# Kernel tuning notes

Hardware: AMD Instinct MI355X
Metric: run time of the kernel (lower is better)

Reference implementation:

```python
import jax, jax.numpy as jnp
import numpy as np

B = 65536
IN_F = 1024
OUT_F = 1024


def setup_inputs() -> dict:
    key = jax.random.key(0)
    k1, k2 = jax.random.split(key)
    x = jax.random.normal(k1, (B, IN_F), dtype=jnp.float32)
    # init matches torch: normal(0, sqrt(2/(in+out)))
    std = np.sqrt(2.0 / (IN_F + OUT_F)).astype(np.float32)
    weight = jax.random.normal(k2, (OUT_F, IN_F), dtype=jnp.float32) * std
    bias = jnp.zeros((OUT_F,), dtype=jnp.float32)
    return {"x": x, "weight": weight, "bias": bias}


def reference(x, weight, bias):
    # Deterministic binarization: sign(w) in {-1, 0, +1} (sign(0)=0, same as torch)
    w_bin = jnp.sign(weight)
    # [B, in] @ [in, out] + [out]
    return jnp.matmul(x, w_bin.T) + bias[None, :]
```

## Files before the change

kernel.cpp:

```cpp
#include <hip/hip_runtime.h>


typedef __bf16 bf16x8 __attribute__((ext_vector_type(8)));
typedef float  f32x4  __attribute__((ext_vector_type(4)));

constexpr int Mdim = 65536, Ndim = 1024, Kdim = 1024;
constexpr int BM = 128, BN = 256, BK = 32;
constexpr int NKT = Kdim / BK;
constexpr int NWG = (Mdim / BM) * (Ndim / BN);
constexpr int AROWB = 80;

typedef const __attribute__((address_space(1))) char ga_char;
typedef __attribute__((address_space(3))) char lds_char;
__device__ __forceinline__ void gload16(const void* g, void* l) {
    __builtin_amdgcn_global_load_lds((ga_char*)g, (lds_char*)l, 16, 0, 0);
}
__device__ __forceinline__ f32x4 mfma16(bf16x8 a, bf16x8 b, f32x4 c) {
    return __builtin_amdgcn_mfma_f32_16x16x32_bf16(a, b, c, 0, 0, 0);
}

__global__ __launch_bounds__(256)
void wprep_kernel(const float* __restrict__ W, __bf16* __restrict__ WS) {
    const int id   = blockIdx.x * 256 + threadIdx.x;
    const int colb = id >> 15;
    const int kt   = (id >> 10) & 31;
    const int g    = id & 1023;
    const int nb   = g >> 6;
    const int lane = g & 63;
    const int row  = colb * 256 + nb * 16 + (lane & 15);
    const int col  = kt * 32 + (lane >> 4) * 8;
    const float* src = W + (size_t)row * Kdim + col;
    f32x4 a = *(const f32x4*)src;
    f32x4 b = *(const f32x4*)(src + 4);
    bf16x8 o;
#pragma unroll
    for (int e = 0; e < 4; ++e) {
        o[e]     = (__bf16)(float)((a[e] > 0.f) - (a[e] < 0.f));
        o[e + 4] = (__bf16)(float)((b[e] > 0.f) - (b[e] < 0.f));
    }
    *(bf16x8*)(WS + (size_t)id * 8) = o;
}

__global__ __launch_bounds__(512, 4)
void binlin128x256(const float* __restrict__ X, const __bf16* __restrict__ WS,
                   const float* __restrict__ bias, float* __restrict__ out)
{
    __shared__ __align__(16) char Al[2][BM * AROWB];
    __shared__ __align__(16) __bf16 Bl[2][BN * BK];

    const int swz  = (blockIdx.x & 7) * (NWG / 8) + (blockIdx.x >> 3);
    const int colb = swz & 3;
    const int rowb = swz >> 2;
    const int row0 = rowb * BM;

    const int tid  = threadIdx.x;
    const int lane = tid & 63;
    const int wid  = tid >> 6;
    const int wr   = wid >> 2;
    const int wcn  = wid & 3;
    const int fr   = lane & 15;
    const int hq   = lane >> 4;

    const int a_r = tid >> 2;
    const int a_c = (tid & 3) * 8;
    const float* Xb = X + (size_t)(row0 + a_r) * Kdim + a_c;

    const __bf16* WSb = WS + (size_t)colb * (Ndim / BN == 4 ? 262144 : 262144);

    f32x4 ra[2];
    auto GLA = [&](int kt) {
        const float* p = Xb + kt * BK;
        ra[0] = *(const f32x4*)p;
        ra[1] = *(const f32x4*)(p + 4);
    };
    auto DSWA = [&](int buf) {
        bf16x8 v;
#pragma unroll
        for (int e = 0; e < 4; ++e) {
            v[e]     = (__bf16)ra[0][e];
            v[e + 4] = (__bf16)ra[1][e];
        }
        *(bf16x8*)(&Al[buf][a_r * AROWB + a_c * 2]) = v;
    };
    auto GLB = [&](int buf, int kt) {
        const __bf16* s = WSb + (size_t)kt * 8192 + wid * 1024 + lane * 8;
        gload16(s,       &Bl[buf][wid * 1024]);
        gload16(s + 512, &Bl[buf][wid * 1024 + 512]);
    };

    auto lda = [&](int buf, int i) -> bf16x8 {
        const int row = wr * 64 + i * 16 + fr;
        return *(const bf16x8*)(&Al[buf][row * AROWB + hq * 16]);
    };
    auto ldb = [&](int buf, int j) -> bf16x8 {
        const int nb = wcn * 4 + j;
        return *(const bf16x8*)(&Bl[buf][nb * 512 + lane * 8]);
    };

    f32x4 acc[4][4] = {};

    GLA(0); GLB(0, 0); DSWA(0);
    __syncthreads();

    int cur = 0;
    for (int t = 0; t < NKT; ++t) {
        const int nxt = cur ^ 1;
        const bool pre = (t + 1 < NKT);
        if (pre) { GLA(t + 1); GLB(nxt, t + 1); }

        bf16x8 af[4];
#pragma unroll
        for (int i = 0; i < 4; ++i) af[i] = lda(cur, i);
        __builtin_amdgcn_s_setprio(1);
#pragma unroll
        for (int j = 0; j < 4; ++j) {
            bf16x8 bf = ldb(cur, j);
#pragma unroll
            for (int i = 0; i < 4; ++i)
                acc[i][j] = mfma16(af[i], bf, acc[i][j]);
        }
        __builtin_amdgcn_s_setprio(0);

        if (pre) {
            DSWA(nxt);
            __syncthreads();
        }
        cur = nxt;
    }

    const int orow = row0 + wr * 64 + hq * 4;
    const int ocol = colb * BN + wcn * 64 + fr;
#pragma unroll
    for (int j = 0; j < 4; ++j) {
        const float bv = bias[ocol + j * 16];
#pragma unroll
        for (int i = 0; i < 4; ++i)
#pragma unroll
            for (int r = 0; r < 4; ++r)
                out[(size_t)(orow + i * 16 + r) * Ndim + (ocol + j * 16)] =
                    acc[i][j][r] + bv;
    }
}

__global__ __launch_bounds__(256)
void binlin_fallback(const float* __restrict__ X, const float* __restrict__ Wf,
                     const float* __restrict__ bias, float* __restrict__ out)
{
    __shared__ __align__(16) __bf16 Al[2][128][32];
    __shared__ __align__(16) __bf16 Bl[2][128][32];
    constexpr int NT = Kdim / 32;
    const int swz  = (blockIdx.x & 7) * (4096 / 8) + (blockIdx.x >> 3);
    const int colb = swz & 7, rowb = swz >> 3;
    const int row0 = rowb * 128, col0 = colb * 128;
    const int tid = threadIdx.x, lane = tid & 63, wid = tid >> 6;
    const int wr = wid >> 1, wc = wid & 1;
    const int sr = tid >> 2, sc = (tid & 3) * 8;
    const float* Xb = X + (size_t)row0 * Kdim;
    const float* Wb = Wf + (size_t)col0 * Kdim;
    f32x4 ra[2][2], rb[2][2];
    auto GL = [&](int k0) {
#pragma unroll
        for (int p = 0; p < 2; ++p) {
            const float* sa = Xb + (size_t)(p * 64 + sr) * Kdim + k0 + sc;
            ra[p][0] = *(const f32x4*)sa; ra[p][1] = *(const f32x4*)(sa + 4);
            const float* sb = Wb + (size_t)(p * 64 + sr) * Kdim + k0 + sc;
            rb[p][0] = *(const f32x4*)sb; rb[p][1] = *(const f32x4*)(sb + 4);
        }
    };
    auto DSW = [&](int buf) {
#pragma unroll
        for (int p = 0; p < 2; ++p) {
            bf16x8 va, vb;
#pragma unroll
            for (int e = 0; e < 4; ++e) {
                va[e] = (__bf16)ra[p][0][e]; va[e + 4] = (__bf16)ra[p][1][e];
                float a = rb[p][0][e], b = rb[p][1][e];
                vb[e] = (__bf16)(float)((a > 0.f) - (a < 0.f));
                vb[e + 4] = (__bf16)(float)((b > 0.f) - (b < 0.f));
            }
            *(bf16x8*)&Al[buf][p * 64 + sr][sc] = va;
            *(bf16x8*)&Bl[buf][p * 64 + sr][sc] = vb;
        }
    };
    f32x4 acc[4][4] = {};
    const int fr = lane & 15, ks = (lane >> 4) * 8;
    auto COMP = [&](int buf) {
        bf16x8 af[4], bf[4];
#pragma unroll
        for (int i = 0; i < 4; ++i) af[i] = *(const bf16x8*)&Al[buf][wr * 64 + fr + i * 16][ks];
#pragma unroll
        for (int j = 0; j < 4; ++j) bf[j] = *(const bf16x8*)&Bl[buf][wc * 64 + fr + j * 16][ks];
#pragma unroll
        for (int i = 0; i < 4; ++i)
#pragma unroll
            for (int j = 0; j < 4; ++j)
                acc[i][j] = mfma16(af[i], bf[j], acc[i][j]);
    };
    GL(0); DSW(0); __syncthreads();
    int cur = 0;
    for (int t = 0; t < NT; ++t) {
        if (t + 1 < NT) GL((t + 1) * 32);
        COMP(cur);
        if (t + 1 < NT) { DSW(cur ^ 1); __syncthreads(); cur ^= 1; }
    }
    const int orow = row0 + wr * 64 + (lane >> 4) * 4;
    const int ocol = col0 + wc * 64 + fr;
#pragma unroll
    for (int j = 0; j < 4; ++j) {
        const float bv = bias[ocol + j * 16];
#pragma unroll
        for (int i = 0; i < 4; ++i)
#pragma unroll
            for (int r = 0; r < 4; ++r)
                out[(size_t)(orow + i * 16 + r) * Ndim + (ocol + j * 16)] = acc[i][j][r] + bv;
    }
}

extern "C" void kernel_launch(void* const* d_in, const int* in_sizes, int n_in,
                              void* d_out, int out_size, void* d_ws, size_t ws_size,
                              hipStream_t stream) {
    const float* x  = (const float*)d_in[0];
    const float* w  = (const float*)d_in[1];
    const float* b  = (const float*)d_in[2];
    float* out      = (float*)d_out;

    constexpr size_t WS_BYTES = (size_t)Ndim * Kdim * sizeof(__bf16);

    if (ws_size >= WS_BYTES) {
        __bf16* ws = (__bf16*)d_ws;
        wprep_kernel<<<dim3(512), dim3(256), 0, stream>>>(w, ws);
        binlin128x256<<<dim3(NWG), dim3(512), 0, stream>>>(x, ws, b, out);
    } else {
        binlin_fallback<<<dim3(4096), dim3(256), 0, stream>>>(x, w, b, out);
    }
}
```

Before: 233.5 us.

## Prefetch X two tiles ahead and store A in MFMA fragment order

The A operand (X rows) is now loaded from global memory two k-tiles ahead into a double register stage, while B is still fetched one tile ahead through direct-to-LDS loads. The end-of-iteration __syncthreads is replaced by explicit waitcnt on LDS and on vector memory (leaving two loads outstanding), plus a raw s_barrier, so the X prefetch can stay in flight across the barrier. The A tile in LDS moves from a padded row layout to MFMA fragment order, so each lane reads one contiguous 16-byte chunk. The extra register stage raises register pressure, and the hand-written vmcnt value depends on the compiler's load ordering, which makes correctness fragile.

```diff
diff --git a/kernel.cpp b/kernel.cpp
--- a/kernel.cpp
+++ b/kernel.cpp
@@ -8,7 +8,6 @@
 constexpr int BM = 128, BN = 256, BK = 32;
 constexpr int NKT = Kdim / BK;
 constexpr int NWG = (Mdim / BM) * (Ndim / BN);
-constexpr int AROWB = 80;
 
 typedef const __attribute__((address_space(1))) char ga_char;
 typedef __attribute__((address_space(3))) char lds_char;
@@ -18,6 +17,9 @@
 __device__ __forceinline__ f32x4 mfma16(bf16x8 a, bf16x8 b, f32x4 c) {
     return __builtin_amdgcn_mfma_f32_16x16x32_bf16(a, b, c, 0, 0, 0);
 }
+#define SBARRIER()   asm volatile("s_barrier" ::: "memory")
+#define WAIT_LGKM0() asm volatile("s_waitcnt lgkmcnt(0)" ::: "memory")
+#define WAIT_VM2()   asm volatile("s_waitcnt vmcnt(2)" ::: "memory")
 
 __global__ __launch_bounds__(256)
 void wprep_kernel(const float* __restrict__ W, __bf16* __restrict__ WS) {
@@ -42,10 +44,10 @@
 }
 
 __global__ __launch_bounds__(512, 4)
-void binlin128x256(const float* __restrict__ X, const __bf16* __restrict__ WS,
-                   const float* __restrict__ bias, float* __restrict__ out)
+void binlin_d2(const float* __restrict__ X, const __bf16* __restrict__ WS,
+               const float* __restrict__ bias, float* __restrict__ out)
 {
-    __shared__ __align__(16) char Al[2][BM * AROWB];
+    __shared__ __align__(16) __bf16 Al[2][BM * BK];
     __shared__ __align__(16) __bf16 Bl[2][BN * BK];
 
     const int swz  = (blockIdx.x & 7) * (NWG / 8) + (blockIdx.x >> 3);
@@ -61,26 +63,25 @@
     const int fr   = lane & 15;
     const int hq   = lane >> 4;
 
-    const int a_r = tid >> 2;
-    const int a_c = (tid & 3) * 8;
-    const float* Xb = X + (size_t)(row0 + a_r) * Kdim + a_c;
-
-    const __bf16* WSb = WS + (size_t)colb * (Ndim / BN == 4 ? 262144 : 262144);
-
-    f32x4 ra[2];
-    auto GLA = [&](int kt) {
-        const float* p = Xb + kt * BK;
-        ra[0] = *(const f32x4*)p;
-        ra[1] = *(const f32x4*)(p + 4);
-    };
-    auto DSWA = [&](int buf) {
+    const float* Xs = X + (size_t)(row0 + wid * 16 + fr) * Kdim + hq * 8;
+    const int a_dst = (wid * 64 + lane) * 8;
+
+    const __bf16* WSb = WS + (size_t)colb * 262144;
+
+    f32x4 rA[2][2];
+    auto GLA = [&](int kt, int s) {
+        const float* p = Xs + kt * BK;
+        rA[s][0] = *(const f32x4*)p;
+        rA[s][1] = *(const f32x4*)(p + 4);
+    };
+    auto DSWA = [&](int buf, int s) {
         bf16x8 v;
 #pragma unroll
         for (int e = 0; e < 4; ++e) {
-            v[e]     = (__bf16)ra[0][e];
-            v[e + 4] = (__bf16)ra[1][e];
-        }
-        *(bf16x8*)(&Al[buf][a_r * AROWB + a_c * 2]) = v;
+            v[e]     = (__bf16)rA[s][0][e];
+            v[e + 4] = (__bf16)rA[s][1][e];
+        }
+        *(bf16x8*)(&Al[buf][a_dst]) = v;
     };
     auto GLB = [&](int buf, int kt) {
         const __bf16* s = WSb + (size_t)kt * 8192 + wid * 1024 + lane * 8;
@@ -89,24 +90,28 @@
     };
 
     auto lda = [&](int buf, int i) -> bf16x8 {
-        const int row = wr * 64 + i * 16 + fr;
-        return *(const bf16x8*)(&Al[buf][row * AROWB + hq * 16]);
+        return *(const bf16x8*)(&Al[buf][((wr * 4 + i) * 64 + lane) * 8]);
     };
     auto ldb = [&](int buf, int j) -> bf16x8 {
-        const int nb = wcn * 4 + j;
-        return *(const bf16x8*)(&Bl[buf][nb * 512 + lane * 8]);
+        return *(const bf16x8*)(&Bl[buf][((wcn * 4 + j) * 64 + lane) * 8]);
     };
 
     f32x4 acc[4][4] = {};
 
-    GLA(0); GLB(0, 0); DSWA(0);
+    GLB(0, 0);
+    GLA(0, 0);
+    GLA(1, 1);
+    DSWA(0, 0);
     __syncthreads();
 
-    int cur = 0;
     for (int t = 0; t < NKT; ++t) {
+        const int cur = t & 1;
         const int nxt = cur ^ 1;
-        const bool pre = (t + 1 < NKT);
-        if (pre) { GLA(t + 1); GLB(nxt, t + 1); }
+        const int tB  = (t + 1 < NKT) ? t + 1 : NKT - 1;
+        const int tA  = (t + 2 < NKT) ? t + 2 : NKT - 1;
+
+        GLB(nxt, tB);
+        GLA(tA, cur);
 
         bf16x8 af[4];
 #pragma unroll
@@ -121,11 +126,11 @@
         }
         __builtin_amdgcn_s_setprio(0);
 
-        if (pre) {
-            DSWA(nxt);
-            __syncthreads();
-        }
-        cur = nxt;
+        DSWA(nxt, nxt);
+        WAIT_LGKM0();
+        WAIT_VM2();
+        __builtin_amdgcn_sched_barrier(0);
+        SBARRIER();
     }
 
     const int orow = row0 + wr * 64 + hq * 4;
@@ -229,7 +234,7 @@
     if (ws_size >= WS_BYTES) {
         __bf16* ws = (__bf16*)d_ws;
         wprep_kernel<<<dim3(512), dim3(256), 0, stream>>>(w, ws);
-        binlin128x256<<<dim3(NWG), dim3(512), 0, stream>>>(x, ws, b, out);
+        binlin_d2<<<dim3(NWG), dim3(512), 0, stream>>>(x, ws, b, out);
     } else {
         binlin_fallback<<<dim3(4096), dim3(256), 0, stream>>>(x, w, b, out);
     }
```

Result: slower. 246.6 us (+5.6%).

## Pre-convert X to bf16 MFMA layout and use 256x256 four-stage ring GEMM

Applied to the files above, without the earlier changes.

Adds an xprep kernel that converts X to bf16 in a fragment-ordered layout, so the main GEMM can stream both operands with global_load_lds straight into LDS. The new main kernel uses 256x256 tiles, a 4-slot LDS ring with prefetch depth 3, and split-phase barriers. This removes the in-loop fp32 register loads and conversion of X and raises arithmetic intensity per tile. In exchange it adds a full extra pass that reads the fp32 X and writes a bf16 copy (128 MB workspace), and it lowers occupancy to 2 workgroups per CU.

```diff
diff --git a/kernel.cpp b/kernel.cpp
--- a/kernel.cpp
+++ b/kernel.cpp
@@ -5,10 +5,9 @@
 typedef float  f32x4  __attribute__((ext_vector_type(4)));
 
 constexpr int Mdim = 65536, Ndim = 1024, Kdim = 1024;
-constexpr int BM = 128, BN = 256, BK = 32;
+constexpr int BM = 256, BN = 256, BK = 32;
 constexpr int NKT = Kdim / BK;
 constexpr int NWG = (Mdim / BM) * (Ndim / BN);
-constexpr int AROWB = 80;
 
 typedef const __attribute__((address_space(1))) char ga_char;
 typedef __attribute__((address_space(3))) char lds_char;
@@ -20,38 +19,55 @@
 }
 
 __global__ __launch_bounds__(256)
-void wprep_kernel(const float* __restrict__ W, __bf16* __restrict__ WS) {
+void xprep_kernel(const float* __restrict__ X, __bf16* __restrict__ XB) {
     const int id   = blockIdx.x * 256 + threadIdx.x;
-    const int colb = id >> 15;
+    const int l    = id & 63;
+    const int mb   = (id >> 6) & 15;
     const int kt   = (id >> 10) & 31;
-    const int g    = id & 1023;
-    const int nb   = g >> 6;
-    const int lane = g & 63;
-    const int row  = colb * 256 + nb * 16 + (lane & 15);
-    const int col  = kt * 32 + (lane >> 4) * 8;
-    const float* src = W + (size_t)row * Kdim + col;
+    const int rowb = id >> 15;
+    const float* src = X + (size_t)(rowb * 256 + mb * 16 + (l & 15)) * Kdim
+                         + kt * 32 + (l >> 4) * 8;
     f32x4 a = *(const f32x4*)src;
     f32x4 b = *(const f32x4*)(src + 4);
     bf16x8 o;
 #pragma unroll
     for (int e = 0; e < 4; ++e) {
+        o[e]     = (__bf16)a[e];
+        o[e + 4] = (__bf16)b[e];
+    }
+    *(bf16x8*)(XB + (size_t)id * 8) = o;
+}
+
+__global__ __launch_bounds__(256)
+void wprep_kernel(const float* __restrict__ W, __bf16* __restrict__ WB) {
+    const int id   = blockIdx.x * 256 + threadIdx.x;
+    const int l    = id & 63;
+    const int nb   = (id >> 6) & 15;
+    const int kt   = (id >> 10) & 31;
+    const int colb = id >> 15;
+    const float* src = W + (size_t)(colb * 256 + nb * 16 + (l & 15)) * Kdim
+                         + kt * 32 + (l >> 4) * 8;
+    f32x4 a = *(const f32x4*)src;
+    f32x4 b = *(const f32x4*)(src + 4);
+    bf16x8 o;
+#pragma unroll
+    for (int e = 0; e < 4; ++e) {
         o[e]     = (__bf16)(float)((a[e] > 0.f) - (a[e] < 0.f));
         o[e + 4] = (__bf16)(float)((b[e] > 0.f) - (b[e] < 0.f));
     }
-    *(bf16x8*)(WS + (size_t)id * 8) = o;
-}
-
-__global__ __launch_bounds__(512, 4)
-void binlin128x256(const float* __restrict__ X, const __bf16* __restrict__ WS,
-                   const float* __restrict__ bias, float* __restrict__ out)
+    *(bf16x8*)(WB + (size_t)id * 8) = o;
+}
+
+__global__ __launch_bounds__(512, 2)
+void binlin_ring(const __bf16* __restrict__ XB, const __bf16* __restrict__ WB,
+                 const float* __restrict__ bias, float* __restrict__ out)
 {
-    __shared__ __align__(16) char Al[2][BM * AROWB];
-    __shared__ __align__(16) __bf16 Bl[2][BN * BK];
+    __shared__ __align__(16) __bf16 Al[4][8192];
+    __shared__ __align__(16) __bf16 Bl[4][8192];
 
     const int swz  = (blockIdx.x & 7) * (NWG / 8) + (blockIdx.x >> 3);
     const int colb = swz & 3;
     const int rowb = swz >> 2;
-    const int row0 = rowb * BM;
 
     const int tid  = threadIdx.x;
     const int lane = tid & 63;
@@ -61,15 +77,101 @@
     const int fr   = lane & 15;
     const int hq   = lane >> 4;
 
+    const char* XAb = (const char*)(XB + (size_t)rowb * 32 * 8192);
+    const char* WBb = (const char*)(WB + (size_t)colb * 32 * 8192);
+
+    auto stage = [&](int slot, int ktc, int half) {
+        const int off = half * 8192 + wid * 1024;
+        gload16(XAb + ktc * 16384 + off + lane * 16, (char*)&Al[slot][0] + off);
+        gload16(WBb + ktc * 16384 + off + lane * 16, (char*)&Bl[slot][0] + off);
+    };
+
+    const int aoff = (wr * 8 * 64 + lane) * 16;
+    const int boff = (wcn * 4 * 64 + lane) * 16;
+
+    f32x4 acc[8][4] = {};
+
+#pragma unroll
+    for (int tt = 0; tt < 3; ++tt) { stage(tt, tt, 0); stage(tt, tt, 1); }
+    asm volatile("s_waitcnt vmcnt(8)" ::: "memory");
+    __builtin_amdgcn_s_barrier();
+
+    for (int t = 0; t < NKT; ++t) {
+        const int slotC = t & 3;
+        const int slotS = (t + 3) & 3;
+        const int ktc   = (t + 3 < NKT) ? t + 3 : NKT - 1;
+        const char* A = (const char*)&Al[slotC][0];
+        const char* B = (const char*)&Bl[slotC][0];
+        bf16x8 af[4], bf[4];
+
+        stage(slotS, ktc, 0);
+#pragma unroll
+        for (int j = 0; j < 4; ++j) bf[j] = *(const bf16x8*)(B + boff + j * 1024);
+#pragma unroll
+        for (int i = 0; i < 4; ++i) af[i] = *(const bf16x8*)(A + aoff + i * 1024);
+        __builtin_amdgcn_s_setprio(1);
+#pragma unroll
+        for (int i = 0; i < 4; ++i)
+#pragma unroll
+            for (int j = 0; j < 4; ++j)
+                acc[i][j] = mfma16(af[i], bf[j], acc[i][j]);
+        __builtin_amdgcn_s_setprio(0);
+        __builtin_amdgcn_s_barrier();
+
+        stage(slotS, ktc, 1);
+#pragma unroll
+        for (int i = 0; i < 4; ++i) af[i] = *(const bf16x8*)(A + aoff + (4 + i) * 1024);
+        __builtin_amdgcn_s_setprio(1);
+#pragma unroll
+        for (int i = 0; i < 4; ++i)
+#pragma unroll
+            for (int j = 0; j < 4; ++j)
+                acc[4 + i][j] = mfma16(af[i], bf[j], acc[4 + i][j]);
+        __builtin_amdgcn_s_setprio(0);
+        asm volatile("s_waitcnt vmcnt(8)" ::: "memory");
+        __builtin_amdgcn_s_barrier();
+    }
+
+    const int orow = rowb * 256 + wr * 128 + hq * 4;
+    const int ocol = colb * 256 + wcn * 64 + fr;
+#pragma unroll
+    for (int j = 0; j < 4; ++j) {
+        const float bv = bias[ocol + j * 16];
+#pragma unroll
+        for (int i = 0; i < 8; ++i)
+#pragma unroll
+            for (int r = 0; r < 4; ++r)
+                out[(size_t)(orow + i * 16 + r) * Ndim + (ocol + j * 16)] =
+                    acc[i][j][r] + bv;
+    }
+}
+
+__global__ __launch_bounds__(512, 4)
+void binlin128x256(const float* __restrict__ X, const __bf16* __restrict__ WS,
+                   const float* __restrict__ bias, float* __restrict__ out)
+{
+    constexpr int mBM = 128, mBN = 256, mBK = 32;
+    constexpr int mNWG = (Mdim / mBM) * (Ndim / mBN);
+    __shared__ __align__(16) char Alc[2][mBM * 80];
+    __shared__ __align__(16) __bf16 Bl[2][mBN * mBK];
+    const int swz  = (blockIdx.x & 7) * (mNWG / 8) + (blockIdx.x >> 3);
+    const int colb = swz & 3;
+    const int rowb = swz >> 2;
+    const int row0 = rowb * mBM;
+    const int tid  = threadIdx.x;
+    const int lane = tid & 63;
+    const int wid  = tid >> 6;
+    const int wr   = wid >> 2;
+    const int wcn  = wid & 3;
+    const int fr   = lane & 15;
+    const int hq   = lane >> 4;
     const int a_r = tid >> 2;
     const int a_c = (tid & 3) * 8;
     const float* Xb = X + (size_t)(row0 + a_r) * Kdim + a_c;
-
-    const __bf16* WSb = WS + (size_t)colb * (Ndim / BN == 4 ? 262144 : 262144);
-
+    const __bf16* WSb = WS + (size_t)colb * 262144;
     f32x4 ra[2];
     auto GLA = [&](int kt) {
-        const float* p = Xb + kt * BK;
+        const float* p = Xb + kt * mBK;
         ra[0] = *(const f32x4*)p;
         ra[1] = *(const f32x4*)(p + 4);
     };
@@ -77,59 +179,47 @@
         bf16x8 v;
 #pragma unroll
         for (int e = 0; e < 4; ++e) {
-            v[e]     = (__bf16)ra[0][e];
-            v[e + 4] = (__bf16)ra[1][e];
+            v[e] = (__bf16)ra[0][e]; v[e + 4] = (__bf16)ra[1][e];
         }
-        *(bf16x8*)(&Al[buf][a_r * AROWB + a_c * 2]) = v;
+        *(bf16x8*)(&Alc[buf][a_r * 80 + a_c * 2]) = v;
     };
     auto GLB = [&](int buf, int kt) {
         const __bf16* s = WSb + (size_t)kt * 8192 + wid * 1024 + lane * 8;
         gload16(s,       &Bl[buf][wid * 1024]);
         gload16(s + 512, &Bl[buf][wid * 1024 + 512]);
     };
-
     auto lda = [&](int buf, int i) -> bf16x8 {
         const int row = wr * 64 + i * 16 + fr;
-        return *(const bf16x8*)(&Al[buf][row * AROWB + hq * 16]);
+        return *(const bf16x8*)(&Alc[buf][row * 80 + hq * 16]);
     };
     auto ldb = [&](int buf, int j) -> bf16x8 {
-        const int nb = wcn * 4 + j;
-        return *(const bf16x8*)(&Bl[buf][nb * 512 + lane * 8]);
-    };
-
+        return *(const bf16x8*)(&Bl[buf][(wcn * 4 + j) * 512 + lane * 8]);
+    };
     f32x4 acc[4][4] = {};
-
     GLA(0); GLB(0, 0); DSWA(0);
     __syncthreads();
-
     int cur = 0;
     for (int t = 0; t < NKT; ++t) {
         const int nxt = cur ^ 1;
         const bool pre = (t + 1 < NKT);
         if (pre) { GLA(t + 1); GLB(nxt, t + 1); }
-
         bf16x8 af[4];
 #pragma unroll
         for (int i = 0; i < 4; ++i) af[i] = lda(cur, i);
         __builtin_amdgcn_s_setprio(1);
 #pragma unroll
         for (int j = 0; j < 4; ++j) {
-            bf16x8 bf = ldb(cur, j);
+            bf16x8 bfr = ldb(cur, j);
 #pragma unroll
             for (int i = 0; i < 4; ++i)
-                acc[i][j] = mfma16(af[i], bf, acc[i][j]);
+                acc[i][j] = mfma16(af[i], bfr, acc[i][j]);
         }
         __builtin_amdgcn_s_setprio(0);
-
-        if (pre) {
-            DSWA(nxt);
-            __syncthreads();
-        }
+        if (pre) { DSWA(nxt); __syncthreads(); }
         cur = nxt;
     }
-
     const int orow = row0 + wr * 64 + hq * 4;
-    const int ocol = colb * BN + wcn * 64 + fr;
+    const int ocol = colb * mBN + wcn * 64 + fr;
 #pragma unroll
     for (int j = 0; j < 4; ++j) {
         const float bv = bias[ocol + j * 16];
@@ -224,12 +314,19 @@
     const float* b  = (const float*)d_in[2];
     float* out      = (float*)d_out;
 
-    constexpr size_t WS_BYTES = (size_t)Ndim * Kdim * sizeof(__bf16);
-
-    if (ws_size >= WS_BYTES) {
-        __bf16* ws = (__bf16*)d_ws;
-        wprep_kernel<<<dim3(512), dim3(256), 0, stream>>>(w, ws);
-        binlin128x256<<<dim3(NWG), dim3(512), 0, stream>>>(x, ws, b, out);
+    constexpr size_t WB_BYTES = (size_t)Ndim * Kdim * sizeof(__bf16);
+    constexpr size_t XB_BYTES = (size_t)Mdim * Kdim * sizeof(__bf16);
+
+    if (ws_size >= WB_BYTES + XB_BYTES) {
+        __bf16* wb = (__bf16*)d_ws;
+        __bf16* xb = (__bf16*)((char*)d_ws + WB_BYTES);
+        wprep_kernel<<<dim3(512),   dim3(256), 0, stream>>>(w, wb);
+        xprep_kernel<<<dim3(32768), dim3(256), 0, stream>>>(x, xb);
+        binlin_ring<<<dim3(NWG), dim3(512), 0, stream>>>(xb, wb, b, out);
+    } else if (ws_size >= WB_BYTES) {
+        __bf16* wb = (__bf16*)d_ws;
+        wprep_kernel<<<dim3(512), dim3(256), 0, stream>>>(w, wb);
+        binlin128x256<<<dim3(2048), dim3(512), 0, stream>>>(x, wb, b, out);
     } else {
         binlin_fallback<<<dim3(4096), dim3(256), 0, stream>>>(x, w, b, out);
     }
```

New measurement: 388.7 us. 1.66x slower.
